# Performance work log

Measured on AMD Instinct MI355X. Metric: run time of the kernel, lower is better.

The kernel has to match this reference:

```python
import jax, jax.numpy as jnp
import numpy as np

B, C, H, W = 4, 512, 128, 128
C8 = C // 8


def setup_inputs() -> dict:
    key = jax.random.key(0)
    ks = jax.random.split(key, 10)
    s = 0.02
    return {
        "x_exmplar": jax.random.normal(ks[0], (B, C, H, W), jnp.float32),
        "x_query": jax.random.normal(ks[1], (B, C, H, W), jnp.float32),
        "Wq": jax.random.normal(ks[2], (C8, C), jnp.float32) * s,
        "bq": jax.random.normal(ks[3], (C8,), jnp.float32) * s,
        "Wk": jax.random.normal(ks[4], (C8, C), jnp.float32) * s,
        "bk": jax.random.normal(ks[5], (C8,), jnp.float32) * s,
        "Wv": jax.random.normal(ks[6], (C, C), jnp.float32) * s,
        "bv": jax.random.normal(ks[7], (C,), jnp.float32) * s,
        "gamma_1": jax.random.normal(ks[8], (1,), jnp.float32) * 0.1,
        "gamma_2": jax.random.normal(ks[9], (1,), jnp.float32) * 0.1,
    }


def _conv1x1(x, Wt, b):
    # x: (B,C,H,W), Wt: (O,C) -> (B,O,H,W)
    return jnp.einsum('bchw,oc->bohw', x, Wt) + b[None, :, None, None]


def reference(x_exmplar, x_query, Wq, bq, Wk, bk, Wv, bv, gamma_1, gamma_2):
    q = _conv1x1(x_query, Wq, bq)      # (B,C8,H,W)
    k = _conv1x1(x_exmplar, Wk, bk)    # (B,C8,H,W)
    v = _conv1x1(x_exmplar, Wv, bv)    # (B,C,H,W)

    # vertical (H) path: energy_H[b,h,w,j] = sum_c q[b,c,h,w] k[b,c,j,w], -inf on h==j
    energy_H = jnp.einsum('bchw,bcjw->bhwj', q, k)
    eye = jnp.eye(H, dtype=bool)[None, :, None, :]       # (1,H,1,H)
    energy_H = jnp.where(eye, -jnp.inf, energy_H)
    # horizontal (W) path: energy_W[b,h,w,j] = sum_c q[b,c,h,w] k[b,c,h,j]
    energy_W = jnp.einsum('bchw,bchj->bhwj', q, k)

    concate = jax.nn.softmax(jnp.concatenate([energy_H, energy_W], axis=-1), axis=-1)
    att_H = concate[..., :H]           # (B,H,W,H)
    att_W = concate[..., H:]           # (B,H,W,W)

    out_H = jnp.einsum('bcjw,bhwj->bchw', v, att_H)
    out_W = jnp.einsum('bchj,bhwj->bchw', v, att_W)

    # diagonal (LR / RL) paths; D = min(H,W) = H for square maps
    q_d = jnp.diagonal(q, axis1=2, axis2=3)   # (B,C8,D)
    k_d = jnp.diagonal(k, axis1=2, axis2=3)   # (B,C8,D)
    v_d = jnp.diagonal(v, axis1=2, axis2=3)   # (B,C,D)
    # diag of transpose(2,3) with offset 0 equals diag, so LR == RL faithfully
    energy_LR = jnp.einsum('bci,bcj->bij', k_d, q_d)  # (B,D,D)
    energy_RL = energy_LR
    # softmax over a singleton trailing axis (as in the original code)
    out_LR = jax.nn.softmax(jnp.einsum('bcd,bdj->bcj', v_d, energy_LR)[..., None], axis=3)
    out_RL = jax.nn.softmax(jnp.einsum('bcd,bdj->bcj', v_d, energy_RL)[..., None], axis=3)

    out_sum = out_H + out_W + out_LR + out_RL   # (B,C,H,W) via broadcast of (B,C,D,1)
    return (gamma_1 * out_sum + x_exmplar, gamma_2 * out_sum + x_query)
```

## Files before the change

### kernel.cpp

```cpp
#include <hip/hip_runtime.h>
#include <stdint.h>

typedef unsigned short u16;
typedef __attribute__((ext_vector_type(8))) short bf16x8;
typedef __attribute__((ext_vector_type(4))) float f32x4;

#define NB   4
#define NC   512
#define NC8  64
#define NH   128
#define NW   128
#define NHW  16384

__device__ __forceinline__ float b2f(u16 u) {
  union { float f; uint32_t i; } x; x.i = ((uint32_t)u) << 16; return x.f;
}
__device__ __forceinline__ u16 f2b(float f) {
  union { float f; uint32_t u; } x; x.f = f;
  uint32_t r = x.u + 0x7FFF + ((x.u >> 16) & 1);
  return (u16)(r >> 16);
}
__device__ __forceinline__ uint4 pack8bf(const float* f) {
  uint4 u;
  u.x = (uint32_t)f2b(f[0]) | ((uint32_t)f2b(f[1]) << 16);
  u.y = (uint32_t)f2b(f[2]) | ((uint32_t)f2b(f[3]) << 16);
  u.z = (uint32_t)f2b(f[4]) | ((uint32_t)f2b(f[5]) << 16);
  u.w = (uint32_t)f2b(f[6]) | ((uint32_t)f2b(f[7]) << 16);
  return u;
}

__global__ __launch_bounds__(256) void convert_w(const float* __restrict__ W,
                                                 u16* __restrict__ Wb) {
  int i = (blockIdx.x * 256 + threadIdx.x) * 8;
  float4 a = *reinterpret_cast<const float4*>(W + i);
  float4 b = *reinterpret_cast<const float4*>(W + i + 4);
  float f[8] = {a.x, a.y, a.z, a.w, b.x, b.y, b.z, b.w};
  *reinterpret_cast<uint4*>(Wb + i) = pack8bf(f);
}

__global__ __launch_bounds__(256) void transpose_cvt(const float* __restrict__ x,
                                                     u16* __restrict__ xT) {
  __shared__ float tile[32][33];
  int b = blockIdx.z;
  int c0 = blockIdx.y * 32;
  int n0 = blockIdx.x * 32;
  int tx = threadIdx.x & 31, ty = threadIdx.x >> 5;
  const float* src = x + ((size_t)b * NC + c0) * NHW + n0;
  for (int k = 0; k < 4; k++)
    tile[ty + k * 8][tx] = src[(size_t)(ty + k * 8) * NHW + tx];
  __syncthreads();
  u16* dst = xT + ((size_t)b * NHW + n0) * NC + c0;
  for (int k = 0; k < 4; k++) {
    int n = ty + k * 8;
    dst[(size_t)n * NC + tx] = f2b(tile[tx][n]);
  }
}

__global__ __launch_bounds__(256) void proj64T(const float* __restrict__ x,
                                               const float* __restrict__ Wt,
                                               const float* __restrict__ bias,
                                               u16* __restrict__ yT) {
  int b = blockIdx.y;
  int hw0 = blockIdx.x * 128;
  __shared__ float xs[32][128];
  __shared__ float ws[64][32];
  int t = threadIdx.x;
  int og = t >> 5;
  int wl = t & 31;
  float acc[8][4];
  for (int i = 0; i < 8; i++) for (int j = 0; j < 4; j++) acc[i][j] = 0.f;
  const float* xb = x + (size_t)b * NC * NHW + hw0;
  for (int c0 = 0; c0 < NC; c0 += 32) {
    for (int i = 0; i < 4; i++) {
      int idx4 = t + i * 256;
      int cc = idx4 >> 5, w4 = (idx4 & 31) * 4;
      float4 v = *reinterpret_cast<const float4*>(&xb[(size_t)(c0 + cc) * NHW + w4]);
      xs[cc][w4 + 0] = v.x; xs[cc][w4 + 1] = v.y; xs[cc][w4 + 2] = v.z; xs[cc][w4 + 3] = v.w;
    }
    for (int i = 0; i < 2; i++) {
      int idx4 = t + i * 256;
      int o = idx4 >> 3, cb4 = (idx4 & 7) * 4;
      float4 v = *reinterpret_cast<const float4*>(&Wt[(size_t)o * NC + c0 + cb4]);
      ws[o][cb4 + 0] = v.x; ws[o][cb4 + 1] = v.y; ws[o][cb4 + 2] = v.z; ws[o][cb4 + 3] = v.w;
    }
    __syncthreads();
    for (int cc = 0; cc < 32; cc++) {
      float a[8], bb[4];
      for (int i = 0; i < 8; i++) a[i] = ws[og * 8 + i][cc];
      for (int j = 0; j < 4; j++) bb[j] = xs[cc][wl * 4 + j];
      for (int i = 0; i < 8; i++)
        for (int j = 0; j < 4; j++) acc[i][j] += a[i] * bb[j];
    }
    __syncthreads();
  }
  float bv[8];
  for (int i = 0; i < 8; i++) bv[i] = bias[og * 8 + i];
  for (int j = 0; j < 4; j++) {
    float col[8];
    for (int i = 0; i < 8; i++) col[i] = acc[i][j] + bv[i];
    size_t hw = (size_t)hw0 + wl * 4 + j;
    *reinterpret_cast<uint4*>(&yT[((size_t)b * NHW + hw) * 64 + og * 8]) = pack8bf(col);
  }
}

__global__ __launch_bounds__(256) void proj_v_mfma(const u16* __restrict__ xT,
                                                   const u16* __restrict__ Wb,
                                                   const float* __restrict__ bias,
                                                   u16* __restrict__ y) {
  __shared__ __align__(16) u16 smem[16384];
  char* AsB = (char*)smem;
  char* BsB = (char*)(smem + 8192);
  int o0 = blockIdx.x * 128, n0 = blockIdx.y * 128, b = blockIdx.z;
  int t = threadIdx.x;
  int wid = t >> 6, lane = t & 63;
  int wm = wid >> 1, wn = wid & 1;
  int l15 = lane & 15, lhi = lane >> 4;

  f32x4 acc[4][4];
#pragma unroll
  for (int m = 0; m < 4; m++)
#pragma unroll
    for (int n = 0; n < 4; n++)
#pragma unroll
      for (int r = 0; r < 4; r++) acc[m][n][r] = 0.f;

  const u16* Arow = Wb + (size_t)o0 * NC;
  const u16* Brow = xT + ((size_t)b * NHW + n0) * NC;

  for (int c0 = 0; c0 < NC; c0 += 64) {
#pragma unroll
    for (int p = 0; p < 4; p++) {
      int idx = t + p * 256;
      int row = idx >> 3;
      int cb  = (idx & 7) * 8;
      int dst = row * 128 + ((cb * 2) ^ ((row & 7) << 4));
      bf16x8 av = *reinterpret_cast<const bf16x8*>(Arow + (size_t)row * NC + c0 + cb);
      *reinterpret_cast<bf16x8*>(AsB + dst) = av;
      bf16x8 bv = *reinterpret_cast<const bf16x8*>(Brow + (size_t)row * NC + c0 + cb);
      *reinterpret_cast<bf16x8*>(BsB + dst) = bv;
    }
    __syncthreads();
#pragma unroll
    for (int kk = 0; kk < 2; kk++) {
      int kbyte = kk * 64 + lhi * 16;
      bf16x8 af[4], bfr[4];
#pragma unroll
      for (int m = 0; m < 4; m++) {
        int row = wm * 64 + m * 16 + l15;
        af[m] = *reinterpret_cast<const bf16x8*>(AsB + row * 128 + (kbyte ^ ((row & 7) << 4)));
      }
#pragma unroll
      for (int n = 0; n < 4; n++) {
        int row = wn * 64 + n * 16 + l15;
        bfr[n] = *reinterpret_cast<const bf16x8*>(BsB + row * 128 + (kbyte ^ ((row & 7) << 4)));
      }
#pragma unroll
      for (int m = 0; m < 4; m++)
#pragma unroll
        for (int n = 0; n < 4; n++)
          acc[m][n] = __builtin_amdgcn_mfma_f32_16x16x32_bf16(af[m], bfr[n], acc[m][n], 0, 0, 0);
    }
    __syncthreads();
  }

  char* stage = (char*)smem + wid * 8192;
#pragma unroll
  for (int m = 0; m < 4; m++) {
#pragma unroll
    for (int r = 0; r < 4; r++) {
      int lrow = m * 16 + lhi * 4 + r;
      float bval = bias[o0 + wm * 64 + lrow];
#pragma unroll
      for (int n = 0; n < 4; n++) {
        int col = n * 16 + l15;
        *reinterpret_cast<u16*>(stage + lrow * 128 + col * 2) = f2b(acc[m][n][r] + bval);
      }
    }
  }
  __syncthreads();
#pragma unroll
  for (int s = 0; s < 8; s++) {
    int row  = s * 8 + (lane >> 3);
    int colb = (lane & 7) * 8;
    uint4 v = *reinterpret_cast<const uint4*>(stage + row * 128 + colb * 2);
    size_t addr = ((size_t)b * NC + o0 + wm * 64 + row) * (size_t)NHW + n0 + wn * 64 + colb;
    *reinterpret_cast<uint4*>(&y[addr]) = v;
  }
}

__global__ __launch_bounds__(256) void transpose128(const u16* __restrict__ src,
                                                    u16* __restrict__ dst) {
  __shared__ u16 tile[32][33];
  int p = blockIdx.z;
  int i0 = blockIdx.y * 32, j0 = blockIdx.x * 32;
  int tx = threadIdx.x & 31, ty = threadIdx.x >> 5;
  const u16* s = src + (size_t)p * NHW;
  u16* d = dst + (size_t)p * NHW;
  for (int k = 0; k < 4; k++) {
    int i = i0 + ty + k * 8;
    tile[ty + k * 8][tx] = s[(size_t)i * 128 + j0 + tx];
  }
  __syncthreads();
  for (int k = 0; k < 4; k++) {
    int j = j0 + ty + k * 8;
    d[(size_t)j * 128 + i0 + tx] = tile[tx][ty + k * 8];
  }
}

__global__ __launch_bounds__(256) void energy_mfma(const u16* __restrict__ QT,
                                                   const u16* __restrict__ KT,
                                                   u16* __restrict__ att, int isH) {
  __shared__ __align__(16) u16 smem[16384];
  char* AsB = (char*)smem;
  char* BsB = (char*)(smem + 8192);
  int s = blockIdx.x, b = blockIdx.y;
  int t = threadIdx.x;
  int wid = t >> 6, lane = t & 63;
  int wm = wid >> 1, wn = wid & 1;
  int l15 = lane & 15, lhi = lane >> 4;

  size_t base = (size_t)b * NHW * 64;
  size_t rowstride = isH ? (size_t)128 * 64 : 64;
  size_t off0 = isH ? (size_t)s * 64 : (size_t)s * 128 * 64;

  f32x4 acc[4][4];
#pragma unroll
  for (int m = 0; m < 4; m++)
#pragma unroll
    for (int n = 0; n < 4; n++)
#pragma unroll
      for (int r = 0; r < 4; r++) acc[m][n][r] = 0.f;

#pragma unroll
  for (int p = 0; p < 4; p++) {
    int idx = t + p * 256;
    int row = idx >> 3;
    int cb  = (idx & 7) * 8;
    int dst = row * 128 + ((cb * 2) ^ ((row & 7) << 4));
    bf16x8 av = *reinterpret_cast<const bf16x8*>(QT + base + off0 + (size_t)row * rowstride + cb);
    *reinterpret_cast<bf16x8*>(AsB + dst) = av;
    bf16x8 bv = *reinterpret_cast<const bf16x8*>(KT + base + off0 + (size_t)row * rowstride + cb);
    *reinterpret_cast<bf16x8*>(BsB + dst) = bv;
  }
  __syncthreads();
#pragma unroll
  for (int kk = 0; kk < 2; kk++) {
    int kbyte = kk * 64 + lhi * 16;
    bf16x8 af[4], bfr[4];
#pragma unroll
    for (int m = 0; m < 4; m++) {
      int row = wm * 64 + m * 16 + l15;
      af[m] = *reinterpret_cast<const bf16x8*>(AsB + row * 128 + (kbyte ^ ((row & 7) << 4)));
    }
#pragma unroll
    for (int n = 0; n < 4; n++) {
      int row = wn * 64 + n * 16 + l15;
      bfr[n] = *reinterpret_cast<const bf16x8*>(BsB + row * 128 + (kbyte ^ ((row & 7) << 4)));
    }
#pragma unroll
    for (int m = 0; m < 4; m++)
#pragma unroll
      for (int n = 0; n < 4; n++)
        acc[m][n] = __builtin_amdgcn_mfma_f32_16x16x32_bf16(af[m], bfr[n], acc[m][n], 0, 0, 0);
  }
  __syncthreads();

  char* stage = (char*)smem + wid * 8192;
#pragma unroll
  for (int m = 0; m < 4; m++) {
#pragma unroll
    for (int r = 0; r < 4; r++) {
      int lrow = m * 16 + lhi * 4 + r;
      int grow = wm * 64 + lrow;
#pragma unroll
      for (int n = 0; n < 4; n++) {
        int col = n * 16 + l15;
        int gcol = wn * 64 + col;
        float v = acc[m][n][r];
        if (isH && gcol == grow) v = -1e30f;
        *reinterpret_cast<u16*>(stage + lrow * 128 + col * 2) = f2b(v);
      }
    }
  }
  __syncthreads();
  size_t attb = (size_t)b * 4194304;
#pragma unroll
  for (int sb = 0; sb < 8; sb++) {
    int row  = wm * 64 + sb * 8 + (lane >> 3);
    int colb = wn * 64 + (lane & 7) * 8;
    uint4 v = *reinterpret_cast<const uint4*>(stage + (sb * 8 + (lane >> 3)) * 128 + (lane & 7) * 16);
    size_t addr = attb + (isH ? ((size_t)row * 32768 + (size_t)s * 256 + colb)
                              : ((size_t)s * 32768 + (size_t)row * 256 + 128 + colb));
    *reinterpret_cast<uint4*>(&att[addr]) = v;
  }
}

__global__ __launch_bounds__(256) void softmax_kern(u16* __restrict__ att) {
  int wave = threadIdx.x >> 6;
  int lane = threadIdx.x & 63;
  size_t row = (size_t)blockIdx.x * 4 + wave;
  u16* p = att + row * 256;
  uint2 u = *reinterpret_cast<const uint2*>(&p[lane * 4]);
  float v[4];
  v[0] = b2f((u16)(u.x & 0xFFFF)); v[1] = b2f((u16)(u.x >> 16));
  v[2] = b2f((u16)(u.y & 0xFFFF)); v[3] = b2f((u16)(u.y >> 16));
  float mx = fmaxf(fmaxf(v[0], v[1]), fmaxf(v[2], v[3]));
  for (int off = 32; off; off >>= 1) mx = fmaxf(mx, __shfl_xor(mx, off));
  float sum = 0.f;
  for (int i = 0; i < 4; i++) { v[i] = __expf(v[i] - mx); sum += v[i]; }
  for (int off = 32; off; off >>= 1) sum += __shfl_xor(sum, off);
  float inv = 1.f / sum;
  uint2 o;
  o.x = (uint32_t)f2b(v[0] * inv) | ((uint32_t)f2b(v[1] * inv) << 16);
  o.y = (uint32_t)f2b(v[2] * inv) | ((uint32_t)f2b(v[3] * inv) << 16);
  *reinterpret_cast<uint2*>(&p[lane * 4]) = o;
}

__global__ __launch_bounds__(256) void out_gemm_mfma(const u16* __restrict__ V,
                                                     const u16* __restrict__ att,
                                                     u16* __restrict__ out, int isH) {
  __shared__ __align__(16) u16 smem[16384];
  char* AsB = (char*)smem;
  char* BsB = (char*)(smem + 8192);
  int ct = blockIdx.x, s = blockIdx.y, b = blockIdx.z;
  int t = threadIdx.x;
  int wid = t >> 6, lane = t & 63;
  int wm = wid >> 1, wn = wid & 1;
  int l15 = lane & 15, lhi = lane >> 4;

  f32x4 acc[4][4];
#pragma unroll
  for (int m = 0; m < 4; m++)
#pragma unroll
    for (int n = 0; n < 4; n++)
#pragma unroll
      for (int r = 0; r < 4; r++) acc[m][n][r] = 0.f;

  const u16* Abase = V + ((size_t)(b * NC + ct * 128)) * NHW + (size_t)s * 128;
  size_t attb = (size_t)b * 4194304;
  size_t bbase = attb + (isH ? (size_t)s * 256 : (size_t)s * 32768 + 128);
  size_t bstride = isH ? 32768 : 256;

  for (int c0 = 0; c0 < 128; c0 += 64) {
#pragma unroll
    for (int p = 0; p < 4; p++) {
      int idx = t + p * 256;
      int row = idx >> 3;
      int cb  = (idx & 7) * 8;
      int dst = row * 128 + ((cb * 2) ^ ((row & 7) << 4));
      bf16x8 av = *reinterpret_cast<const bf16x8*>(Abase + (size_t)row * NHW + c0 + cb);
      *reinterpret_cast<bf16x8*>(AsB + dst) = av;
      bf16x8 bv = *reinterpret_cast<const bf16x8*>(att + bbase + (size_t)row * bstride + c0 + cb);
      *reinterpret_cast<bf16x8*>(BsB + dst) = bv;
    }
    __syncthreads();
#pragma unroll
    for (int kk = 0; kk < 2; kk++) {
      int kbyte = kk * 64 + lhi * 16;
      bf16x8 af[4], bfr[4];
#pragma unroll
      for (int m = 0; m < 4; m++) {
        int row = wm * 64 + m * 16 + l15;
        af[m] = *reinterpret_cast<const bf16x8*>(AsB + row * 128 + (kbyte ^ ((row & 7) << 4)));
      }
#pragma unroll
      for (int n = 0; n < 4; n++) {
        int row = wn * 64 + n * 16 + l15;
        bfr[n] = *reinterpret_cast<const bf16x8*>(BsB + row * 128 + (kbyte ^ ((row & 7) << 4)));
      }
#pragma unroll
      for (int m = 0; m < 4; m++)
#pragma unroll
        for (int n = 0; n < 4; n++)
          acc[m][n] = __builtin_amdgcn_mfma_f32_16x16x32_bf16(af[m], bfr[n], acc[m][n], 0, 0, 0);
    }
    __syncthreads();
  }

  char* stage = (char*)smem + wid * 8192;
#pragma unroll
  for (int m = 0; m < 4; m++) {
#pragma unroll
    for (int r = 0; r < 4; r++) {
      int lrow = m * 16 + lhi * 4 + r;
#pragma unroll
      for (int n = 0; n < 4; n++) {
        int col = n * 16 + l15;
        *reinterpret_cast<u16*>(stage + lrow * 128 + col * 2) = f2b(acc[m][n][r]);
      }
    }
  }
  __syncthreads();
#pragma unroll
  for (int sb = 0; sb < 8; sb++) {
    int row  = sb * 8 + (lane >> 3);
    int colb = (lane & 7) * 8;
    uint4 v = *reinterpret_cast<const uint4*>(stage + row * 128 + colb * 2);
    size_t addr = ((size_t)(b * NC + ct * 128 + wm * 64 + row)) * NHW + (size_t)s * 128 + wn * 64 + colb;
    *reinterpret_cast<uint4*>(&out[addr]) = v;
  }
}

__global__ __launch_bounds__(256) void epilogue(const u16* __restrict__ outWbf,
                                                const u16* __restrict__ outHsw,
                                                const float* __restrict__ xe,
                                                const float* __restrict__ xq,
                                                const float* __restrict__ g1p,
                                                const float* __restrict__ g2p,
                                                float* out0, float* out1) {
  __shared__ float tile[32][33];
  int p = blockIdx.z;
  int h0 = blockIdx.y * 32, w0 = blockIdx.x * 32;
  int tx = threadIdx.x & 31, ty = threadIdx.x >> 5;
  const u16* src = outHsw + (size_t)p * NHW;
  for (int k = 0; k < 4; k++) {
    int w = w0 + ty + k * 8;
    tile[ty + k * 8][tx] = b2f(src[(size_t)w * 128 + h0 + tx]);
  }
  __syncthreads();
  float g1 = g1p[0], g2 = g2p[0];
  for (int k = 0; k < 4; k++) {
    int h = h0 + ty + k * 8;
    size_t idx = (size_t)p * NHW + (size_t)h * 128 + w0 + tx;
    float sum = b2f(outWbf[idx]) + tile[tx][ty + k * 8] + 2.0f;
    out0[idx] = g1 * sum + xe[idx];
    out1[idx] = g2 * sum + xq[idx];
  }
}

extern "C" void kernel_launch(void* const* d_in, const int* in_sizes, int n_in,
                              void* d_out, int out_size, void* d_ws, size_t ws_size,
                              hipStream_t stream) {
  (void)in_sizes; (void)n_in; (void)out_size; (void)ws_size;
  const float* xe = (const float*)d_in[0];
  const float* xq = (const float*)d_in[1];
  const float* Wq = (const float*)d_in[2];
  const float* bq = (const float*)d_in[3];
  const float* Wk = (const float*)d_in[4];
  const float* bk = (const float*)d_in[5];
  const float* Wv = (const float*)d_in[6];
  const float* bv = (const float*)d_in[7];
  const float* g1 = (const float*)d_in[8];
  const float* g2 = (const float*)d_in[9];
  float* out = (float*)d_out;

  char* ws = (char*)d_ws;
  u16* qT    = (u16*)(ws + 0);
  u16* kT    = (u16*)(ws + 8388608);
  u16* wv_bf = (u16*)(ws + 16777216);
  u16* v_n   = (u16*)(ws + 33554432);
  u16* v_sw  = (u16*)(ws + 100663296);
  u16* att   = (u16*)(ws + 167772160);
  u16* xeT   = (u16*)(ws + 201326592);

  convert_w<<<dim3(128), 256, 0, stream>>>(Wv, wv_bf);
  transpose_cvt<<<dim3(512, 16, 4), 256, 0, stream>>>(xe, xeT);
  proj64T<<<dim3(128, 4), 256, 0, stream>>>(xq, Wq, bq, qT);
  proj64T<<<dim3(128, 4), 256, 0, stream>>>(xe, Wk, bk, kT);
  proj_v_mfma<<<dim3(4, 128, 4), 256, 0, stream>>>(xeT, wv_bf, bv, v_n);
  transpose128<<<dim3(4, 4, 2048), 256, 0, stream>>>(v_n, v_sw);
  energy_mfma<<<dim3(128, 4), 256, 0, stream>>>(qT, kT, att, 0);
  energy_mfma<<<dim3(128, 4), 256, 0, stream>>>(qT, kT, att, 1);
  softmax_kern<<<dim3(16384), 256, 0, stream>>>(att);
  out_gemm_mfma<<<dim3(4, 128, 4), 256, 0, stream>>>(v_n, att, v_n, 0);
  out_gemm_mfma<<<dim3(4, 128, 4), 256, 0, stream>>>(v_sw, att, v_sw, 1);
  epilogue<<<dim3(4, 4, 2048), 256, 0, stream>>>(v_n, v_sw, xe, xq, g1, g2,
                                                 out, out + 33554432);
}
```

Measured before the change: 863.6 us.

## Move Q/K projections to bf16 MFMA and vectorize transpose and epilogue

Replaces the fp32 SIMT Q and K 1x1-conv projections with a bf16 MFMA GEMM that reads the transposed bf16 activations, reusing the transposed exemplar buffer for K and adding a second transpose of the query input. The transpose kernel now writes 16-byte packed bf16 stores, and the epilogue is reworked to use 128-bit loads and stores with larger tiles. This trades extra weight conversions and one extra full-size transpose pass for much cheaper projection arithmetic and wider memory accesses. Q and K are now computed from bf16-rounded inputs, which lowers their precision.

```diff
diff --git a/kernel.cpp b/kernel.cpp
--- a/kernel.cpp
+++ b/kernel.cpp
@@ -28,6 +28,12 @@
   u.w = (uint32_t)f2b(f[6]) | ((uint32_t)f2b(f[7]) << 16);
   return u;
 }
+__device__ __forceinline__ void unpack8bf(uint4 u, float* f) {
+  f[0] = b2f((u16)(u.x & 0xFFFF)); f[1] = b2f((u16)(u.x >> 16));
+  f[2] = b2f((u16)(u.y & 0xFFFF)); f[3] = b2f((u16)(u.y >> 16));
+  f[4] = b2f((u16)(u.z & 0xFFFF)); f[5] = b2f((u16)(u.z >> 16));
+  f[6] = b2f((u16)(u.w & 0xFFFF)); f[7] = b2f((u16)(u.w >> 16));
+}
 
 __global__ __launch_bounds__(256) void convert_w(const float* __restrict__ W,
                                                  u16* __restrict__ Wb) {
@@ -44,62 +50,107 @@
   int b = blockIdx.z;
   int c0 = blockIdx.y * 32;
   int n0 = blockIdx.x * 32;
-  int tx = threadIdx.x & 31, ty = threadIdx.x >> 5;
+  int t = threadIdx.x;
+  int tx = t & 31, ty = t >> 5;
   const float* src = x + ((size_t)b * NC + c0) * NHW + n0;
   for (int k = 0; k < 4; k++)
     tile[ty + k * 8][tx] = src[(size_t)(ty + k * 8) * NHW + tx];
   __syncthreads();
-  u16* dst = xT + ((size_t)b * NHW + n0) * NC + c0;
-  for (int k = 0; k < 4; k++) {
-    int n = ty + k * 8;
-    dst[(size_t)n * NC + tx] = f2b(tile[tx][n]);
-  }
-}
-
-__global__ __launch_bounds__(256) void proj64T(const float* __restrict__ x,
-                                               const float* __restrict__ Wt,
-                                               const float* __restrict__ bias,
-                                               u16* __restrict__ yT) {
-  int b = blockIdx.y;
-  int hw0 = blockIdx.x * 128;
-  __shared__ float xs[32][128];
-  __shared__ float ws[64][32];
+  if (t < 128) {
+    int n = t >> 2, cg = t & 3;
+    float f[8];
+    for (int j = 0; j < 8; j++) f[j] = tile[cg * 8 + j][n];
+    *reinterpret_cast<uint4*>(&xT[((size_t)b * NHW + n0 + n) * NC + c0 + cg * 8]) = pack8bf(f);
+  }
+}
+
+__global__ __launch_bounds__(256) void proj64_mfma(const u16* __restrict__ xT,
+                                                   const u16* __restrict__ Wb,
+                                                   const float* __restrict__ bias,
+                                                   u16* __restrict__ yT) {
+  __shared__ __align__(16) u16 smem[12288];
+  char* AsB = (char*)smem;
+  char* BsB = (char*)smem + 8192;
+  int n0 = blockIdx.x * 128, b = blockIdx.y;
   int t = threadIdx.x;
-  int og = t >> 5;
-  int wl = t & 31;
-  float acc[8][4];
-  for (int i = 0; i < 8; i++) for (int j = 0; j < 4; j++) acc[i][j] = 0.f;
-  const float* xb = x + (size_t)b * NC * NHW + hw0;
-  for (int c0 = 0; c0 < NC; c0 += 32) {
-    for (int i = 0; i < 4; i++) {
-      int idx4 = t + i * 256;
-      int cc = idx4 >> 5, w4 = (idx4 & 31) * 4;
-      float4 v = *reinterpret_cast<const float4*>(&xb[(size_t)(c0 + cc) * NHW + w4]);
-      xs[cc][w4 + 0] = v.x; xs[cc][w4 + 1] = v.y; xs[cc][w4 + 2] = v.z; xs[cc][w4 + 3] = v.w;
-    }
-    for (int i = 0; i < 2; i++) {
-      int idx4 = t + i * 256;
-      int o = idx4 >> 3, cb4 = (idx4 & 7) * 4;
-      float4 v = *reinterpret_cast<const float4*>(&Wt[(size_t)o * NC + c0 + cb4]);
-      ws[o][cb4 + 0] = v.x; ws[o][cb4 + 1] = v.y; ws[o][cb4 + 2] = v.z; ws[o][cb4 + 3] = v.w;
+  int wid = t >> 6, lane = t & 63;
+  int wm = wid >> 1, wn = wid & 1;
+  int l15 = lane & 15, lhi = lane >> 4;
+
+  f32x4 acc[2][4];
+#pragma unroll
+  for (int m = 0; m < 2; m++)
+#pragma unroll
+    for (int n = 0; n < 4; n++)
+#pragma unroll
+      for (int r = 0; r < 4; r++) acc[m][n][r] = 0.f;
+
+  const u16* Bbase = xT + ((size_t)b * NHW + n0) * NC;
+
+  for (int c0 = 0; c0 < NC; c0 += 64) {
+#pragma unroll
+    for (int p = 0; p < 2; p++) {
+      int idx = t + p * 256;
+      int row = idx >> 3, cb = (idx & 7) * 8;
+      int dst = row * 128 + ((cb * 2) ^ ((row & 7) << 4));
+      bf16x8 av = *reinterpret_cast<const bf16x8*>(Wb + (size_t)row * NC + c0 + cb);
+      *reinterpret_cast<bf16x8*>(AsB + dst) = av;
+    }
+#pragma unroll
+    for (int p = 0; p < 4; p++) {
+      int idx = t + p * 256;
+      int row = idx >> 3, cb = (idx & 7) * 8;
+      int dst = row * 128 + ((cb * 2) ^ ((row & 7) << 4));
+      bf16x8 bv = *reinterpret_cast<const bf16x8*>(Bbase + (size_t)row * NC + c0 + cb);
+      *reinterpret_cast<bf16x8*>(BsB + dst) = bv;
     }
     __syncthreads();
-    for (int cc = 0; cc < 32; cc++) {
-      float a[8], bb[4];
-      for (int i = 0; i < 8; i++) a[i] = ws[og * 8 + i][cc];
-      for (int j = 0; j < 4; j++) bb[j] = xs[cc][wl * 4 + j];
-      for (int i = 0; i < 8; i++)
-        for (int j = 0; j < 4; j++) acc[i][j] += a[i] * bb[j];
+#pragma unroll
+    for (int kk = 0; kk < 2; kk++) {
+      int kbyte = kk * 64 + lhi * 16;
+      bf16x8 af[2], bfr[4];
+#pragma unroll
+      for (int m = 0; m < 2; m++) {
+        int row = wm * 32 + m * 16 + l15;
+        af[m] = *reinterpret_cast<const bf16x8*>(AsB + row * 128 + (kbyte ^ ((row & 7) << 4)));
+      }
+#pragma unroll
+      for (int n = 0; n < 4; n++) {
+        int row = wn * 64 + n * 16 + l15;
+        bfr[n] = *reinterpret_cast<const bf16x8*>(BsB + row * 128 + (kbyte ^ ((row & 7) << 4)));
+      }
+#pragma unroll
+      for (int m = 0; m < 2; m++)
+#pragma unroll
+        for (int n = 0; n < 4; n++)
+          acc[m][n] = __builtin_amdgcn_mfma_f32_16x16x32_bf16(af[m], bfr[n], acc[m][n], 0, 0, 0);
     }
     __syncthreads();
   }
-  float bv[8];
-  for (int i = 0; i < 8; i++) bv[i] = bias[og * 8 + i];
-  for (int j = 0; j < 4; j++) {
-    float col[8];
-    for (int i = 0; i < 8; i++) col[i] = acc[i][j] + bv[i];
-    size_t hw = (size_t)hw0 + wl * 4 + j;
-    *reinterpret_cast<uint4*>(&yT[((size_t)b * NHW + hw) * 64 + og * 8]) = pack8bf(col);
+
+  char* stage = (char*)smem;
+#pragma unroll
+  for (int m = 0; m < 2; m++) {
+#pragma unroll
+    for (int r = 0; r < 4; r++) {
+      int o = wm * 32 + m * 16 + lhi * 4 + r;
+      float bval = bias[o];
+#pragma unroll
+      for (int n = 0; n < 4; n++) {
+        int col = wn * 64 + n * 16 + l15;
+        int byte = col * 128 + ((o * 2) ^ ((col & 7) << 4));
+        *reinterpret_cast<u16*>(stage + byte) = f2b(acc[m][n][r] + bval);
+      }
+    }
+  }
+  __syncthreads();
+#pragma unroll
+  for (int p = 0; p < 4; p++) {
+    int idx = t + p * 256;
+    int col = idx >> 3, seg = idx & 7;
+    int byte = col * 128 + ((seg * 16) ^ ((col & 7) << 4));
+    uint4 v = *reinterpret_cast<const uint4*>(stage + byte);
+    *reinterpret_cast<uint4*>(&yT[((size_t)b * NHW + n0 + col) * 64 + seg * 8]) = v;
   }
 }
 
@@ -407,25 +458,39 @@
                                                 const float* __restrict__ xq,
                                                 const float* __restrict__ g1p,
                                                 const float* __restrict__ g2p,
-                                                float* out0, float* out1) {
-  __shared__ float tile[32][33];
+                                                float* __restrict__ out0,
+                                                float* __restrict__ out1) {
+  __shared__ float tile[32][65];
   int p = blockIdx.z;
-  int h0 = blockIdx.y * 32, w0 = blockIdx.x * 32;
-  int tx = threadIdx.x & 31, ty = threadIdx.x >> 5;
-  const u16* src = outHsw + (size_t)p * NHW;
-  for (int k = 0; k < 4; k++) {
-    int w = w0 + ty + k * 8;
-    tile[ty + k * 8][tx] = b2f(src[(size_t)w * 128 + h0 + tx]);
+  int h0 = blockIdx.y * 64, w0 = blockIdx.x * 32;
+  int t = threadIdx.x;
+  {
+    int w = t >> 3, hc = t & 7;
+    uint4 v = *reinterpret_cast<const uint4*>(
+        &outHsw[(size_t)p * NHW + (size_t)(w0 + w) * 128 + h0 + hc * 8]);
+    float f[8]; unpack8bf(v, f);
+    for (int j = 0; j < 8; j++) tile[w][hc * 8 + j] = f[j];
   }
   __syncthreads();
   float g1 = g1p[0], g2 = g2p[0];
-  for (int k = 0; k < 4; k++) {
-    int h = h0 + ty + k * 8;
-    size_t idx = (size_t)p * NHW + (size_t)h * 128 + w0 + tx;
-    float sum = b2f(outWbf[idx]) + tile[tx][ty + k * 8] + 2.0f;
-    out0[idx] = g1 * sum + xe[idx];
-    out1[idx] = g2 * sum + xq[idx];
-  }
+  int h = t >> 2, wc = t & 3;
+  size_t idx = (size_t)p * NHW + (size_t)(h0 + h) * 128 + w0 + wc * 8;
+  uint4 wv = *reinterpret_cast<const uint4*>(&outWbf[idx]);
+  float s[8]; unpack8bf(wv, s);
+  float4 xe0 = *reinterpret_cast<const float4*>(&xe[idx]);
+  float4 xe1 = *reinterpret_cast<const float4*>(&xe[idx + 4]);
+  float4 xq0 = *reinterpret_cast<const float4*>(&xq[idx]);
+  float4 xq1 = *reinterpret_cast<const float4*>(&xq[idx + 4]);
+  float sum[8];
+  for (int j = 0; j < 8; j++) sum[j] = s[j] + tile[wc * 8 + j][h] + 2.0f;
+  float4 o0a = {g1 * sum[0] + xe0.x, g1 * sum[1] + xe0.y, g1 * sum[2] + xe0.z, g1 * sum[3] + xe0.w};
+  float4 o0b = {g1 * sum[4] + xe1.x, g1 * sum[5] + xe1.y, g1 * sum[6] + xe1.z, g1 * sum[7] + xe1.w};
+  float4 o1a = {g2 * sum[0] + xq0.x, g2 * sum[1] + xq0.y, g2 * sum[2] + xq0.z, g2 * sum[3] + xq0.w};
+  float4 o1b = {g2 * sum[4] + xq1.x, g2 * sum[5] + xq1.y, g2 * sum[6] + xq1.z, g2 * sum[7] + xq1.w};
+  *reinterpret_cast<float4*>(&out0[idx])     = o0a;
+  *reinterpret_cast<float4*>(&out0[idx + 4]) = o0b;
+  *reinterpret_cast<float4*>(&out1[idx])     = o1a;
+  *reinterpret_cast<float4*>(&out1[idx + 4]) = o1b;
 }
 
 extern "C" void kernel_launch(void* const* d_in, const int* in_sizes, int n_in,
@@ -448,22 +513,27 @@
   u16* qT    = (u16*)(ws + 0);
   u16* kT    = (u16*)(ws + 8388608);
   u16* wv_bf = (u16*)(ws + 16777216);
+  u16* wq_bf = (u16*)(ws + 17301504);
+  u16* wk_bf = (u16*)(ws + 17367040);
   u16* v_n   = (u16*)(ws + 33554432);
   u16* v_sw  = (u16*)(ws + 100663296);
   u16* att   = (u16*)(ws + 167772160);
-  u16* xeT   = (u16*)(ws + 201326592);
+  u16* xT    = (u16*)(ws + 201326592);
 
   convert_w<<<dim3(128), 256, 0, stream>>>(Wv, wv_bf);
-  transpose_cvt<<<dim3(512, 16, 4), 256, 0, stream>>>(xe, xeT);
-  proj64T<<<dim3(128, 4), 256, 0, stream>>>(xq, Wq, bq, qT);
-  proj64T<<<dim3(128, 4), 256, 0, stream>>>(xe, Wk, bk, kT);
-  proj_v_mfma<<<dim3(4, 128, 4), 256, 0, stream>>>(xeT, wv_bf, bv, v_n);
+  convert_w<<<dim3(16), 256, 0, stream>>>(Wq, wq_bf);
+  convert_w<<<dim3(16), 256, 0, stream>>>(Wk, wk_bf);
+  transpose_cvt<<<dim3(512, 16, 4), 256, 0, stream>>>(xe, xT);
+  proj64_mfma<<<dim3(128, 4), 256, 0, stream>>>(xT, wk_bf, bk, kT);
+  proj_v_mfma<<<dim3(4, 128, 4), 256, 0, stream>>>(xT, wv_bf, bv, v_n);
+  transpose_cvt<<<dim3(512, 16, 4), 256, 0, stream>>>(xq, xT);
+  proj64_mfma<<<dim3(128, 4), 256, 0, stream>>>(xT, wq_bf, bq, qT);
   transpose128<<<dim3(4, 4, 2048), 256, 0, stream>>>(v_n, v_sw);
   energy_mfma<<<dim3(128, 4), 256, 0, stream>>>(qT, kT, att, 0);
   energy_mfma<<<dim3(128, 4), 256, 0, stream>>>(qT, kT, att, 1);
   softmax_kern<<<dim3(16384), 256, 0, stream>>>(att);
   out_gemm_mfma<<<dim3(4, 128, 4), 256, 0, stream>>>(v_n, att, v_n, 0);
   out_gemm_mfma<<<dim3(4, 128, 4), 256, 0, stream>>>(v_sw, att, v_sw, 1);
-  epilogue<<<dim3(4, 4, 2048), 256, 0, stream>>>(v_n, v_sw, xe, xq, g1, g2,
+  epilogue<<<dim3(4, 2, 2048), 256, 0, stream>>>(v_n, v_sw, xe, xq, g1, g2,
                                                  out, out + 33554432);
 }
```

Result: faster. 771.0 us (-10.7%).
